# Performance work log

Hardware: AMD Instinct MI355X
Metric: run time of the kernel (lower is better)

## Reference

```python
import jax, jax.numpy as jnp
import numpy as np

N = 50000        # nodes
E = 800000       # random edges (plus N self-loops added in setup)
DIN = 128        # input_dim
H = 128          # hidden_dim
L = 3            # num_layers
EPS = 1e-5       # BatchNorm1d eps


def _bn(x, gamma, beta):
    # BatchNorm1d in training mode: batch stats over node axis, biased variance
    m = x.mean(axis=0)
    v = jnp.mean((x - m) ** 2, axis=0)
    return (x - m) * jax.lax.rsqrt(v + EPS) * gamma + beta


def setup_inputs() -> dict:
    key = jax.random.key(0)
    ks = jax.random.split(key, 11)
    feats = jax.random.normal(ks[0], (N, DIN), dtype=jnp.float32)
    # edge list with self-loops so every node has degree >= 1 (average pooling divides by degree)
    loops = jnp.arange(N, dtype=jnp.int64)
    src = jnp.concatenate([jax.random.randint(ks[1], (E,), 0, N, dtype=jnp.int64), loops])
    dst = jnp.concatenate([jax.random.randint(ks[2], (E,), 0, N, dtype=jnp.int64), loops])
    s = 0.05
    # per-layer MLP params (num_mlp_layers=2: Linear -> BN -> ReLU -> Linear), layer 0 has DIN==H
    W1 = jax.random.normal(ks[3], (L, DIN, H), dtype=jnp.float32) * s
    b1 = jnp.zeros((L, H), jnp.float32)
    g1 = jnp.ones((L, H), jnp.float32)
    be1 = jnp.zeros((L, H), jnp.float32)
    W2 = jax.random.normal(ks[4], (L, H, H), dtype=jnp.float32) * s
    b2 = jnp.zeros((L, H), jnp.float32)
    # outer BatchNorm1d per GNN layer
    og = jnp.ones((L, H), jnp.float32)
    ob = jnp.zeros((L, H), jnp.float32)
    return {"feats": feats, "W1": W1, "b1": b1, "g1": g1, "be1": be1,
            "W2": W2, "b2": b2, "og": og, "ob": ob, "src": src, "dst": dst}


def reference(feats, W1, b1, g1, be1, W2, b2, og, ob, src, dst):
    n = feats.shape[0]
    # degree = spmm(Adj, ones) -- constant across layers
    deg = jax.ops.segment_sum(jnp.ones(src.shape, jnp.float32), dst, num_segments=n)[:, None]
    h = feats
    for l in range(L):
        # pooled = spmm(Adj, h) via edge gather + segment reduce, then 'average' normalize
        pooled = jax.ops.segment_sum(h[src], dst, num_segments=n) / deg
        # GIN-style 2-layer MLP: Linear -> BN -> ReLU -> Linear
        z = jax.nn.relu(_bn(pooled @ W1[l] + b1[l], g1[l], be1[l]))
        z = z @ W2[l] + b2[l]
        # outer BatchNorm + ReLU
        h = jax.nn.relu(_bn(z, og[l], ob[l]))
    return h
```

## Files before the change

kernel.cpp:

```cpp
#include <hip/hip_runtime.h>
#include <hip/hip_bf16.h>
#include <stdint.h>

typedef _Float16 h16;
typedef h16 h16x2 __attribute__((ext_vector_type(2)));
typedef h16 h16x8 __attribute__((ext_vector_type(8)));
typedef float f32x4 __attribute__((ext_vector_type(4)));

#define HF 128
#define EPS 1e-5f
#define BSH 9
#define BROWS 512
#define BCAP 16384
#define ECHUNK 8192
#define SBANKS 8

union pk32 { uint32_t u; h16x2 h; };

static __device__ __forceinline__ uint32_t pack_h16(float a, float b) {
    pk32 c;
    c.h[0] = (h16)a; c.h[1] = (h16)b;
    return c.u;
}

static __device__ __forceinline__ float sum8(const float* __restrict__ st, int idx) {
    float s = 0.f;
#pragma unroll
    for (int b = 0; b < SBANKS; b++) s += st[b * 256 + idx];
    return s;
}


__global__ __launch_bounds__(256) void k_bscatter(const int* __restrict__ src,
                                                  const int* __restrict__ dst,
                                                  int* __restrict__ gcursor,
                                                  int2* __restrict__ staging, int ne, int nb) {
    __shared__ int h[128], gb[128];
    const int tid = threadIdx.x;
    if (tid < nb) h[tid] = 0;
    __syncthreads();
    const int beg = blockIdx.x * ECHUNK;
    const int end = min(beg + ECHUNK, ne);
    for (int i = beg + tid; i < end; i += 256)
        atomicAdd(&h[dst[i] >> BSH], 1);
    __syncthreads();
    if (tid < nb) {
        int c = h[tid];
        gb[tid] = c ? atomicAdd(&gcursor[tid], c) : 0;
        h[tid] = 0;
    }
    __syncthreads();
    for (int i = beg + tid; i < end; i += 256) {
        int d = dst[i];
        int b = d >> BSH;
        int r = atomicAdd(&h[b], 1);
        staging[(size_t)b * BCAP + gb[b] + r] = make_int2(src[i], d);
    }
}

__global__ __launch_bounds__(256) void k_bbuild(const int2* __restrict__ staging,
                                                const int* __restrict__ gcursor,
                                                int* __restrict__ rowbeg,
                                                int* __restrict__ rowend,
                                                float* __restrict__ deginv,
                                                int* __restrict__ csrsrc, int n) {
    __shared__ int hist[BROWS];
    __shared__ int scan[BROWS];
    const int b = blockIdx.x;
    const int tid = threadIdx.x;
    const int rb = b << BSH;
    const int nrows = min(BROWS, n - rb);
    const int base = b * BCAP;
    const int cnt = gcursor[b];
    hist[tid] = 0; hist[tid + 256] = 0;
    __syncthreads();
    for (int i = tid; i < cnt; i += 256)
        atomicAdd(&hist[staging[base + i].y - rb], 1);
    __syncthreads();
    const int i0 = tid, i1 = tid + 256;
    scan[i0] = hist[i0]; scan[i1] = hist[i1];
    __syncthreads();
    for (int off = 1; off < BROWS; off <<= 1) {
        int v0 = (i0 >= off) ? scan[i0 - off] : 0;
        int v1 = (i1 >= off) ? scan[i1 - off] : 0;
        __syncthreads();
        scan[i0] += v0; scan[i1] += v1;
        __syncthreads();
    }
    for (int r = tid; r < BROWS; r += 256) {
        int c = hist[r];
        int excl = scan[r] - c;
        if (r < nrows) {
            rowbeg[rb + r] = base + excl;
            rowend[rb + r] = base + excl + c;
            deginv[rb + r] = c ? 1.0f / (float)c : 0.f;
        }
        scan[r] = excl;
    }
    __syncthreads();
    for (int i = tid; i < cnt; i += 256) {
        int2 e = staging[base + i];
        int pos = atomicAdd(&scan[e.y - rb], 1);
        csrsrc[base + pos] = e.x;
    }
}

__global__ __launch_bounds__(256) void k_prep(const float* __restrict__ W1,
                                              const float* __restrict__ W2,
                                              h16* __restrict__ wp,
                                              const float* __restrict__ feats,
                                              uint32_t* __restrict__ hbuf, long tot2) {
    const int bid = (int)blockIdx.x;
    if (bid < 384) {
        const int mat = bid >> 6;
        const int idx = ((bid & 63) << 8) + (int)threadIdx.x;
        const int l = mat >> 1;
        const float* Wsrc = (mat & 1) ? (W2 + l * 16384) : (W1 + l * 16384);
        const int nn = idx >> 7, k = idx & 127;
        float w = Wsrc[k * 128 + nn];
        int pos = nn * 128 + ((((k >> 3) ^ (nn & 7))) << 3) + (k & 7);
        wp[mat * 16384 + pos] = (h16)w;
    } else {
        long i = (long)(bid - 384) * 256 + threadIdx.x;
        if (i < tot2) {
            float2 v = ((const float2*)feats)[i];
            hbuf[i] = pack_h16(v.x, v.y);
        }
    }
}

template <int AFF>
__global__ __launch_bounds__(256) void k_spmm(const uint32_t* __restrict__ hp,
                                              const int* __restrict__ rowbeg,
                                              const int* __restrict__ rowend,
                                              const float* __restrict__ deginv,
                                              const float* __restrict__ st,
                                              const float* __restrict__ g,
                                              const float* __restrict__ be,
                                              float inv_n,
                                              const int* __restrict__ csrsrc,
                                              uint32_t* __restrict__ pooled, int n, int np) {
    const int wid  = (int)((blockIdx.x * 256u + threadIdx.x) >> 6);
    const int lane = threadIdx.x & 63;
    if (wid >= np) return;
    uint32_t* outp = pooled + (size_t)wid * 64 + lane;
    if (wid >= n) { *outp = 0u; return; }
    h16x2 s2 = (h16x2)(h16)1.f, c2 = (h16x2)(h16)0.f;
    if (AFF) {
        const int c0 = lane * 2, c1 = c0 + 1;
        float m0 = sum8(st, c0) * inv_n, v0 = sum8(st, 128 + c0) * inv_n - m0 * m0;
        float sx = g[c0] * rsqrtf(v0 + EPS), cx = be[c0] - m0 * sx;
        float m1 = sum8(st, c1) * inv_n, v1 = sum8(st, 128 + c1) * inv_n - m1 * m1;
        float sy = g[c1] * rsqrtf(v1 + EPS), cy = be[c1] - m1 * sy;
        s2[0] = (h16)sx; s2[1] = (h16)sy;
        c2[0] = (h16)cx; c2[1] = (h16)cy;
    }
    const h16 z0 = (h16)0.f;
    h16x2 acc = (h16x2)z0;
    const int beg = rowbeg[wid], end = rowend[wid];
    for (int base = beg; base < end; base += 64) {
        const int rem = end - base;
        const int cnt = rem < 64 ? rem : 64;
        const int off = lane < cnt ? lane : cnt - 1;
        const int idx = csrsrc[base + off];
        int j = 0;
        for (; j + 8 <= cnt; j += 8) {
            uint32_t p[8];
#pragma unroll
            for (int u = 0; u < 8; u++) {
                int s = __builtin_amdgcn_readlane(idx, j + u);
                p[u] = hp[(size_t)s * 64 + lane];
            }
#pragma unroll
            for (int u = 0; u < 8; u++) {
                pk32 w; w.u = p[u];
                h16x2 v = w.h;
                if (AFF) {
                    v = v * s2 + c2;
                    v[0] = v[0] > z0 ? v[0] : z0;
                    v[1] = v[1] > z0 ? v[1] : z0;
                }
                acc = acc + v;
            }
        }
        for (; j < cnt; j++) {
            int s = __builtin_amdgcn_readlane(idx, j);
            pk32 w; w.u = hp[(size_t)s * 64 + lane];
            h16x2 v = w.h;
            if (AFF) {
                v = v * s2 + c2;
                v[0] = v[0] > z0 ? v[0] : z0;
                v[1] = v[1] > z0 ? v[1] : z0;
            }
            acc = acc + v;
        }
    }
    const float di = deginv[wid];
    *outp = pack_h16((float)acc[0] * di, (float)acc[1] * di);
}

template <int MODE, int OUTBF>
__global__ __launch_bounds__(256) void k_gemm(const h16* __restrict__ Ah,
                                              const float* __restrict__ Af,
                                              const h16* __restrict__ Wp,
                                              const float* __restrict__ bias,
                                              const float* __restrict__ st,
                                              const float* __restrict__ g,
                                              const float* __restrict__ be,
                                              float inv_n,
                                              float* __restrict__ Yf,
                                              h16* __restrict__ Yb,
                                              float* __restrict__ outstats, int n) {
    __shared__ __align__(16) h16 WT[128 * 128];
    __shared__ float sred[4][128];
    __shared__ float sred2[4][128];
    __shared__ float aff[256];
    const int tid = threadIdx.x;
    const int wave = tid >> 6, lane = tid & 63;

    {
        const char* gsrc = (const char*)Wp + wave * 1024 + lane * 16;
        char* ldst = (char*)&WT[0] + wave * 1024;
#pragma unroll
        for (int i = 0; i < 8; i++) {
            __builtin_amdgcn_global_load_lds(
                (const __attribute__((address_space(1))) uint32_t*)(gsrc + i * 4096),
                (__attribute__((address_space(3))) uint32_t*)(ldst + i * 4096),
                16, 0, 0);
        }
    }
    if (MODE == 1 && tid < 128) {
        float m = sum8(st, tid) * inv_n;
        float v = sum8(st, 128 + tid) * inv_n - m * m;
        float a = g[tid] * rsqrtf(v + EPS);
        aff[tid] = a;
        aff[128 + tid] = be[tid] - m * a;
    }

    const int lrow = lane & 15, quad = lane >> 4;
    const int bx = (int)blockIdx.x * 128;
    int mb[2];
    mb[0] = bx + wave * 16;
    mb[1] = bx + 64 + wave * 16;

    h16x8 ah[2][4];
    if (MODE == 0) {
#pragma unroll
        for (int rt = 0; rt < 2; rt++) {
            const h16* arow = Ah + (size_t)(mb[rt] + lrow) * 128 + quad * 8;
#pragma unroll
            for (int kt = 0; kt < 4; kt++)
                ah[rt][kt] = *(const h16x8*)(arow + kt * 32);
        }
    }

    __syncthreads();

    if (MODE == 1) {
#pragma unroll
        for (int rt = 0; rt < 2; rt++) {
            const float* arow = Af + (size_t)(mb[rt] + lrow) * 128 + quad * 8;
#pragma unroll
            for (int kt = 0; kt < 4; kt++) {
                h16x8 t;
#pragma unroll
                for (int j = 0; j < 8; j++) {
                    int k = kt * 32 + quad * 8 + j;
                    float x = fmaxf(fmaf(arow[kt * 32 + j], aff[k], aff[128 + k]), 0.f);
                    t[j] = (h16)x;
                }
                ah[rt][kt] = t;
            }
        }
    }

    f32x4 acc[2][8];
#pragma unroll
    for (int rt = 0; rt < 2; rt++)
#pragma unroll
        for (int nt = 0; nt < 8; nt++) acc[rt][nt] = (f32x4){0.f, 0.f, 0.f, 0.f};

    const int sw = lrow & 7;
#pragma unroll
    for (int nt = 0; nt < 8; nt++) {
        const h16* wbase = &WT[(nt * 16 + lrow) * 128];
#pragma unroll
        for (int kt = 0; kt < 4; kt++) {
            h16x8 bh = *(const h16x8*)(wbase + (((4 * kt + quad) ^ sw) << 3));
#pragma unroll
            for (int rt = 0; rt < 2; rt++)
                acc[rt][nt] = __builtin_amdgcn_mfma_f32_16x16x32_f16(ah[rt][kt], bh, acc[rt][nt], 0, 0, 0);
        }
    }

#pragma unroll
    for (int nt = 0; nt < 8; nt++) {
        int col = nt * 16 + lrow;
        float bv = bias[col];
        float csum = 0.f, csq = 0.f;
#pragma unroll
        for (int rt = 0; rt < 2; rt++) {
#pragma unroll
            for (int r = 0; r < 4; r++) {
                int row = mb[rt] + quad * 4 + r;
                float yv = acc[rt][nt][r] + bv;
                if (OUTBF) Yb[(size_t)row * 128 + col] = (h16)yv;
                else       Yf[(size_t)row * 128 + col] = yv;
                if (row < n) { csum += yv; csq += yv * yv; }
            }
        }
        csum += __shfl_xor(csum, 16, 64); csum += __shfl_xor(csum, 32, 64);
        csq  += __shfl_xor(csq,  16, 64); csq  += __shfl_xor(csq,  32, 64);
        if (quad == 0) { sred[wave][col] = csum; sred2[wave][col] = csq; }
    }
    __syncthreads();
    if (tid < 128) {
        float s = sred[0][tid] + sred[1][tid] + sred[2][tid] + sred[3][tid];
        float q = sred2[0][tid] + sred2[1][tid] + sred2[2][tid] + sred2[3][tid];
        const int bank = (int)(blockIdx.x & (SBANKS - 1));
        atomicAdd(&outstats[bank * 256 + tid], s);
        atomicAdd(&outstats[bank * 256 + 128 + tid], q);
    }
}

__global__ __launch_bounds__(256) void k_bnrelu(const uint32_t* __restrict__ Z,
                                                const float* __restrict__ st,
                                                const float* __restrict__ g,
                                                const float* __restrict__ be,
                                                float inv_n,
                                                float* __restrict__ out, long tot2) {
    long i = (long)blockIdx.x * 256 + threadIdx.x;
    if (i >= tot2) return;
    int c = (int)((i * 2) & 127);
    float m0 = sum8(st, c) * inv_n,     v0 = sum8(st, 128 + c) * inv_n - m0 * m0;
    float a0 = g[c] * rsqrtf(v0 + EPS),     c0 = be[c] - m0 * a0;
    float m1 = sum8(st, c + 1) * inv_n, v1 = sum8(st, 129 + c) * inv_n - m1 * m1;
    float a1 = g[c + 1] * rsqrtf(v1 + EPS), c1 = be[c + 1] - m1 * a1;
    pk32 w; w.u = Z[i];
    float2 o;
    o.x = fmaxf(fmaf((float)w.h[0], a0, c0), 0.f);
    o.y = fmaxf(fmaf((float)w.h[1], a1, c1), 0.f);
    ((float2*)out)[i] = o;
}

extern "C" void kernel_launch(void* const* d_in, const int* in_sizes, int n_in,
                              void* d_out, int out_size, void* d_ws, size_t ws_size,
                              hipStream_t stream) {
    const float* feats = (const float*)d_in[0];
    const float* W1    = (const float*)d_in[1];
    const float* b1    = (const float*)d_in[2];
    const float* g1    = (const float*)d_in[3];
    const float* be1   = (const float*)d_in[4];
    const float* W2    = (const float*)d_in[5];
    const float* b2    = (const float*)d_in[6];
    const float* og    = (const float*)d_in[7];
    const float* ob    = (const float*)d_in[8];
    const int*   src   = (const int*)d_in[9];
    const int*   dst   = (const int*)d_in[10];

    const int n  = in_sizes[0] / HF;
    const int ne = in_sizes[9];
    const int np = (n + 127) & ~127;
    const int nb = (n + BROWS - 1) >> BSH;

    char* p = (char*)d_ws;
    auto alloc = [&](size_t bytes) -> char* {
        char* r = p;
        p += (bytes + 511) & ~(size_t)511;
        return r;
    };
    uint32_t* hbuf    = (uint32_t*)alloc((size_t)np * 64 * 4);
    uint32_t* pooled  = (uint32_t*)alloc((size_t)np * 64 * 4);
    float*    ybuf    = (float*)   alloc((size_t)np * HF * 4);
    uint32_t* zb      = (uint32_t*)alloc((size_t)np * 64 * 4);
    h16*      wprep   = (h16*)     alloc(6 * 16384 * 2);
    float*    deginv  = (float*)   alloc((size_t)n * 4);
    int*      rowbeg  = (int*)     alloc((size_t)n * 4);
    int*      rowend  = (int*)     alloc((size_t)n * 4);
    int*      csrsrc  = (int*)     alloc((size_t)nb * BCAP * 4);
    int2*     staging = (int2*)    alloc((size_t)nb * BCAP * 8);
    char*     zone    = alloc(512 + 6 * SBANKS * 256 * 4);
    int*      gcursor = (int*)zone;
    float*    stats6  = (float*)(zone + 512);

    hipMemsetAsync(zone, 0, 512 + 6 * SBANKS * 256 * 4, stream);

    const long tot2  = (long)n * (HF / 2);
    const int bnb    = (int)((tot2 + 255) / 256);
    const int spmmb  = np / 4;
    const int gemmb  = np / 128;
    const float inv_n = 1.0f / (float)n;
    const int ebk = (ne + ECHUNK - 1) / ECHUNK;
    const int SL = SBANKS * 256;

    k_prep    <<<384 + bnb, 256, 0, stream>>>(W1, W2, wprep, feats, hbuf, tot2);
    k_bscatter<<<ebk, 256, 0, stream>>>(src, dst, gcursor, staging, ne, nb);
    k_bbuild  <<<nb, 256, 0, stream>>>(staging, gcursor, rowbeg, rowend, deginv, csrsrc, n);

    for (int l = 0; l < 3; l++) {
        float* sY = stats6 + (2 * l) * SL;
        float* sZ = stats6 + (2 * l + 1) * SL;
        if (l == 0)
            k_spmm<0><<<spmmb, 256, 0, stream>>>(hbuf, rowbeg, rowend, deginv,
                                                 nullptr, nullptr, nullptr, inv_n,
                                                 csrsrc, pooled, n, np);
        else
            k_spmm<1><<<spmmb, 256, 0, stream>>>(zb, rowbeg, rowend, deginv,
                                                 stats6 + (2 * (l - 1) + 1) * SL,
                                                 og + (l - 1) * HF, ob + (l - 1) * HF, inv_n,
                                                 csrsrc, pooled, n, np);
        k_gemm<0, 0><<<gemmb, 256, 0, stream>>>((const h16*)pooled, nullptr,
                                                wprep + (size_t)(2 * l) * 16384,
                                                b1 + l * HF,
                                                nullptr, nullptr, nullptr, inv_n,
                                                ybuf, nullptr, sY, n);
        k_gemm<1, 1><<<gemmb, 256, 0, stream>>>(nullptr, ybuf,
                                                wprep + (size_t)(2 * l + 1) * 16384,
                                                b2 + l * HF,
                                                sY, g1 + l * HF, be1 + l * HF, inv_n,
                                                nullptr, (h16*)zb, sZ, n);
    }
    k_bnrelu<<<bnb, 256, 0, stream>>>(zb, stats6 + 5 * SL, og + 2 * HF, ob + 2 * HF,
                                      inv_n, (float*)d_out, tot2);
}
```

Baseline: 370.3 us.

## Fuse two MLP GEMMs into one kernel with grid barrier for BN stats

Merges the first Linear, its BatchNorm+ReLU, and the second Linear into a single kernel. The intermediate Y tile stays in LDS as fp16, and a software grid-wide barrier on an atomic counter waits until the BN statistics from every block are complete. This removes the fp32 Y round-trip through global memory and one kernel launch per layer. It relies on all 391 blocks being co-resident, since launch_bounds(256,2) and 64KB LDS could otherwise deadlock, and Y is now stored at fp16 precision. The SpMM gather loop is also unrolled from 8 to 16 loads in flight.

```diff
diff --git a/kernel.cpp b/kernel.cpp
--- a/kernel.cpp
+++ b/kernel.cpp
@@ -27,6 +27,14 @@
     float s = 0.f;
 #pragma unroll
     for (int b = 0; b < SBANKS; b++) s += st[b * 256 + idx];
+    return s;
+}
+
+static __device__ __forceinline__ float sum8_coh(const float* st, int idx) {
+    float s = 0.f;
+#pragma unroll
+    for (int b = 0; b < SBANKS; b++)
+        s += __hip_atomic_load(&st[b * 256 + idx], __ATOMIC_RELAXED, __HIP_MEMORY_SCOPE_AGENT);
     return s;
 }
 
@@ -164,15 +172,15 @@
         const int off = lane < cnt ? lane : cnt - 1;
         const int idx = csrsrc[base + off];
         int j = 0;
-        for (; j + 8 <= cnt; j += 8) {
-            uint32_t p[8];
-#pragma unroll
-            for (int u = 0; u < 8; u++) {
+        for (; j + 16 <= cnt; j += 16) {
+            uint32_t p[16];
+#pragma unroll
+            for (int u = 0; u < 16; u++) {
                 int s = __builtin_amdgcn_readlane(idx, j + u);
                 p[u] = hp[(size_t)s * 64 + lane];
             }
 #pragma unroll
-            for (int u = 0; u < 8; u++) {
+            for (int u = 0; u < 16; u++) {
                 pk32 w; w.u = p[u];
                 h16x2 v = w.h;
                 if (AFF) {
@@ -199,88 +207,63 @@
     *outp = pack_h16((float)acc[0] * di, (float)acc[1] * di);
 }
 
-template <int MODE, int OUTBF>
-__global__ __launch_bounds__(256) void k_gemm(const h16* __restrict__ Ah,
-                                              const float* __restrict__ Af,
-                                              const h16* __restrict__ Wp,
-                                              const float* __restrict__ bias,
-                                              const float* __restrict__ st,
-                                              const float* __restrict__ g,
-                                              const float* __restrict__ be,
-                                              float inv_n,
-                                              float* __restrict__ Yf,
-                                              h16* __restrict__ Yb,
-                                              float* __restrict__ outstats, int n) {
+__global__ __launch_bounds__(256, 2) void k_mlp(const uint32_t* __restrict__ Ap,
+                                                const h16* __restrict__ Wp1,
+                                                const h16* __restrict__ Wp2,
+                                                const float* __restrict__ b1v,
+                                                const float* __restrict__ b2v,
+                                                const float* __restrict__ g1v,
+                                                const float* __restrict__ be1v,
+                                                float* __restrict__ stY,
+                                                float* __restrict__ stZ,
+                                                float inv_n,
+                                                h16* __restrict__ Z,
+                                                int* __restrict__ ctr, int n) {
     __shared__ __align__(16) h16 WT[128 * 128];
+    __shared__ __align__(16) h16 YT[128 * 128];
     __shared__ float sred[4][128];
     __shared__ float sred2[4][128];
     __shared__ float aff[256];
     const int tid = threadIdx.x;
     const int wave = tid >> 6, lane = tid & 63;
+    const int lrow = lane & 15, quad = lane >> 4;
+    const int bx = (int)blockIdx.x * 128;
+    const int sw = lrow & 7;
+    const int bank = (int)(blockIdx.x & (SBANKS - 1));
 
     {
-        const char* gsrc = (const char*)Wp + wave * 1024 + lane * 16;
+        const char* gsrc = (const char*)Wp1 + wave * 1024 + lane * 16;
         char* ldst = (char*)&WT[0] + wave * 1024;
 #pragma unroll
-        for (int i = 0; i < 8; i++) {
+        for (int i = 0; i < 8; i++)
             __builtin_amdgcn_global_load_lds(
                 (const __attribute__((address_space(1))) uint32_t*)(gsrc + i * 4096),
                 (__attribute__((address_space(3))) uint32_t*)(ldst + i * 4096),
                 16, 0, 0);
-        }
-    }
-    if (MODE == 1 && tid < 128) {
-        float m = sum8(st, tid) * inv_n;
-        float v = sum8(st, 128 + tid) * inv_n - m * m;
-        float a = g[tid] * rsqrtf(v + EPS);
-        aff[tid] = a;
-        aff[128 + tid] = be[tid] - m * a;
-    }
-
-    const int lrow = lane & 15, quad = lane >> 4;
-    const int bx = (int)blockIdx.x * 128;
+    }
+
     int mb[2];
     mb[0] = bx + wave * 16;
     mb[1] = bx + 64 + wave * 16;
 
     h16x8 ah[2][4];
-    if (MODE == 0) {
-#pragma unroll
-        for (int rt = 0; rt < 2; rt++) {
-            const h16* arow = Ah + (size_t)(mb[rt] + lrow) * 128 + quad * 8;
-#pragma unroll
-            for (int kt = 0; kt < 4; kt++)
-                ah[rt][kt] = *(const h16x8*)(arow + kt * 32);
-        }
-    }
-
-    __syncthreads();
-
-    if (MODE == 1) {
-#pragma unroll
-        for (int rt = 0; rt < 2; rt++) {
-            const float* arow = Af + (size_t)(mb[rt] + lrow) * 128 + quad * 8;
-#pragma unroll
-            for (int kt = 0; kt < 4; kt++) {
-                h16x8 t;
-#pragma unroll
-                for (int j = 0; j < 8; j++) {
-                    int k = kt * 32 + quad * 8 + j;
-                    float x = fmaxf(fmaf(arow[kt * 32 + j], aff[k], aff[128 + k]), 0.f);
-                    t[j] = (h16)x;
-                }
-                ah[rt][kt] = t;
-            }
-        }
-    }
+#pragma unroll
+    for (int rt = 0; rt < 2; rt++) {
+        const uint32_t* arow = Ap + (size_t)(mb[rt] + lrow) * 64 + quad * 4;
+#pragma unroll
+        for (int kt = 0; kt < 4; kt++) {
+            uint4 r = *(const uint4*)(arow + kt * 16);
+            ah[rt][kt] = *(const h16x8*)&r;
+        }
+    }
+
+    __syncthreads();
 
     f32x4 acc[2][8];
 #pragma unroll
     for (int rt = 0; rt < 2; rt++)
 #pragma unroll
         for (int nt = 0; nt < 8; nt++) acc[rt][nt] = (f32x4){0.f, 0.f, 0.f, 0.f};
-
-    const int sw = lrow & 7;
 #pragma unroll
     for (int nt = 0; nt < 8; nt++) {
         const h16* wbase = &WT[(nt * 16 + lrow) * 128];
@@ -296,17 +279,16 @@
 #pragma unroll
     for (int nt = 0; nt < 8; nt++) {
         int col = nt * 16 + lrow;
-        float bv = bias[col];
+        float bv = b1v[col];
         float csum = 0.f, csq = 0.f;
 #pragma unroll
         for (int rt = 0; rt < 2; rt++) {
 #pragma unroll
             for (int r = 0; r < 4; r++) {
-                int row = mb[rt] + quad * 4 + r;
+                int lr = wave * 16 + rt * 64 + quad * 4 + r;
                 float yv = acc[rt][nt][r] + bv;
-                if (OUTBF) Yb[(size_t)row * 128 + col] = (h16)yv;
-                else       Yf[(size_t)row * 128 + col] = yv;
-                if (row < n) { csum += yv; csq += yv * yv; }
+                YT[lr * 128 + ((((col >> 3) ^ (lr & 7))) << 3) + (col & 7)] = (h16)yv;
+                if (bx + lr < n) { csum += yv; csq += yv * yv; }
             }
         }
         csum += __shfl_xor(csum, 16, 64); csum += __shfl_xor(csum, 32, 64);
@@ -315,11 +297,95 @@
     }
     __syncthreads();
     if (tid < 128) {
-        float s = sred[0][tid] + sred[1][tid] + sred[2][tid] + sred[3][tid];
-        float q = sred2[0][tid] + sred2[1][tid] + sred2[2][tid] + sred2[3][tid];
-        const int bank = (int)(blockIdx.x & (SBANKS - 1));
-        atomicAdd(&outstats[bank * 256 + tid], s);
-        atomicAdd(&outstats[bank * 256 + 128 + tid], q);
+        atomicAdd(&stY[bank * 256 + tid],       sred[0][tid] + sred[1][tid] + sred[2][tid] + sred[3][tid]);
+        atomicAdd(&stY[bank * 256 + 128 + tid], sred2[0][tid] + sred2[1][tid] + sred2[2][tid] + sred2[3][tid]);
+    }
+    __syncthreads();
+
+    {
+        const char* gsrc = (const char*)Wp2 + wave * 1024 + lane * 16;
+        char* ldst = (char*)&WT[0] + wave * 1024;
+#pragma unroll
+        for (int i = 0; i < 8; i++)
+            __builtin_amdgcn_global_load_lds(
+                (const __attribute__((address_space(1))) uint32_t*)(gsrc + i * 4096),
+                (__attribute__((address_space(3))) uint32_t*)(ldst + i * 4096),
+                16, 0, 0);
+    }
+
+    __threadfence();
+    if (tid == 0) {
+        __hip_atomic_fetch_add(ctr, 1, __ATOMIC_ACQ_REL, __HIP_MEMORY_SCOPE_AGENT);
+        while (__hip_atomic_load(ctr, __ATOMIC_ACQUIRE, __HIP_MEMORY_SCOPE_AGENT) < (int)gridDim.x)
+            __builtin_amdgcn_s_sleep(8);
+    }
+    __syncthreads();
+
+    if (tid < 128) {
+        float m = sum8_coh(stY, tid) * inv_n;
+        float v = sum8_coh(stY, 128 + tid) * inv_n - m * m;
+        float a = g1v[tid] * rsqrtf(v + EPS);
+        aff[tid] = a;
+        aff[128 + tid] = be1v[tid] - m * a;
+    }
+    __syncthreads();
+
+#pragma unroll
+    for (int rt = 0; rt < 2; rt++) {
+#pragma unroll
+        for (int kt = 0; kt < 4; kt++) {
+            int m = wave * 16 + rt * 64 + lrow;
+            h16x8 yv8 = *(const h16x8*)&YT[m * 128 + (((kt * 4 + quad) ^ (m & 7)) << 3)];
+            h16x8 t;
+#pragma unroll
+            for (int j = 0; j < 8; j++) {
+                int k = kt * 32 + quad * 8 + j;
+                float x = fmaxf(fmaf((float)yv8[j], aff[k], aff[128 + k]), 0.f);
+                t[j] = (h16)x;
+            }
+            ah[rt][kt] = t;
+        }
+    }
+
+#pragma unroll
+    for (int rt = 0; rt < 2; rt++)
+#pragma unroll
+        for (int nt = 0; nt < 8; nt++) acc[rt][nt] = (f32x4){0.f, 0.f, 0.f, 0.f};
+#pragma unroll
+    for (int nt = 0; nt < 8; nt++) {
+        const h16* wbase = &WT[(nt * 16 + lrow) * 128];
+#pragma unroll
+        for (int kt = 0; kt < 4; kt++) {
+            h16x8 bh = *(const h16x8*)(wbase + (((4 * kt + quad) ^ sw) << 3));
+#pragma unroll
+            for (int rt = 0; rt < 2; rt++)
+                acc[rt][nt] = __builtin_amdgcn_mfma_f32_16x16x32_f16(ah[rt][kt], bh, acc[rt][nt], 0, 0, 0);
+        }
+    }
+
+#pragma unroll
+    for (int nt = 0; nt < 8; nt++) {
+        int col = nt * 16 + lrow;
+        float bv = b2v[col];
+        float csum = 0.f, csq = 0.f;
+#pragma unroll
+        for (int rt = 0; rt < 2; rt++) {
+#pragma unroll
+            for (int r = 0; r < 4; r++) {
+                int row = mb[rt] + quad * 4 + r;
+                float zv = acc[rt][nt][r] + bv;
+                Z[(size_t)row * 128 + col] = (h16)zv;
+                if (row < n) { csum += zv; csq += zv * zv; }
+            }
+        }
+        csum += __shfl_xor(csum, 16, 64); csum += __shfl_xor(csum, 32, 64);
+        csq  += __shfl_xor(csq,  16, 64); csq  += __shfl_xor(csq,  32, 64);
+        if (quad == 0) { sred[wave][col] = csum; sred2[wave][col] = csq; }
+    }
+    __syncthreads();
+    if (tid < 128) {
+        atomicAdd(&stZ[bank * 256 + tid],       sred[0][tid] + sred[1][tid] + sred[2][tid] + sred[3][tid]);
+        atomicAdd(&stZ[bank * 256 + 128 + tid], sred2[0][tid] + sred2[1][tid] + sred2[2][tid] + sred2[3][tid]);
     }
 }
 
@@ -371,7 +437,6 @@
     };
     uint32_t* hbuf    = (uint32_t*)alloc((size_t)np * 64 * 4);
     uint32_t* pooled  = (uint32_t*)alloc((size_t)np * 64 * 4);
-    float*    ybuf    = (float*)   alloc((size_t)np * HF * 4);
     uint32_t* zb      = (uint32_t*)alloc((size_t)np * 64 * 4);
     h16*      wprep   = (h16*)     alloc(6 * 16384 * 2);
     float*    deginv  = (float*)   alloc((size_t)n * 4);
@@ -379,11 +444,12 @@
     int*      rowend  = (int*)     alloc((size_t)n * 4);
     int*      csrsrc  = (int*)     alloc((size_t)nb * BCAP * 4);
     int2*     staging = (int2*)    alloc((size_t)nb * BCAP * 8);
-    char*     zone    = alloc(512 + 6 * SBANKS * 256 * 4);
+    char*     zone    = alloc(1024 + 6 * SBANKS * 256 * 4);
     int*      gcursor = (int*)zone;
-    float*    stats6  = (float*)(zone + 512);
-
-    hipMemsetAsync(zone, 0, 512 + 6 * SBANKS * 256 * 4, stream);
+    int*      bctr    = (int*)(zone + 512);
+    float*    stats6  = (float*)(zone + 1024);
+
+    hipMemsetAsync(zone, 0, 1024 + 6 * SBANKS * 256 * 4, stream);
 
     const long tot2  = (long)n * (HF / 2);
     const int bnb    = (int)((tot2 + 255) / 256);
@@ -409,16 +475,13 @@
                                                  stats6 + (2 * (l - 1) + 1) * SL,
                                                  og + (l - 1) * HF, ob + (l - 1) * HF, inv_n,
                                                  csrsrc, pooled, n, np);
-        k_gemm<0, 0><<<gemmb, 256, 0, stream>>>((const h16*)pooled, nullptr,
-                                                wprep + (size_t)(2 * l) * 16384,
-                                                b1 + l * HF,
-                                                nullptr, nullptr, nullptr, inv_n,
-                                                ybuf, nullptr, sY, n);
-        k_gemm<1, 1><<<gemmb, 256, 0, stream>>>(nullptr, ybuf,
-                                                wprep + (size_t)(2 * l + 1) * 16384,
-                                                b2 + l * HF,
-                                                sY, g1 + l * HF, be1 + l * HF, inv_n,
-                                                nullptr, (h16*)zb, sZ, n);
+        k_mlp<<<gemmb, 256, 0, stream>>>(pooled,
+                                         wprep + (size_t)(2 * l) * 16384,
+                                         wprep + (size_t)(2 * l + 1) * 16384,
+                                         b1 + l * HF, b2 + l * HF,
+                                         g1 + l * HF, be1 + l * HF,
+                                         sY, sZ, inv_n,
+                                         (h16*)zb, bctr + l, n);
     }
     k_bnrelu<<<bnb, 256, 0, stream>>>(zb, stats6 + 5 * SL, og + 2 * HF, ob + 2 * HF,
                                       inv_n, (float*)d_out, tot2);
```

New measurement: 537.6 us. 45.2% more time.
